# Optimization experiments

Measured on AMD Instinct MI355X. Metric: run time of the kernel, lower is better.

The kernel has to match this reference:

```python
import jax, jax.numpy as jnp
import numpy as np

DIM_EMBED = 256
NUM_DAGS = 1024
OPS_PER_DAG = 100
TOTAL_OPS = NUM_DAGS * OPS_PER_DAG
NUM_WORKERS = 64
H1, H2 = 32, 16


def _mlp_params(key, d_in, scale=0.05):
    ks = jax.random.split(key, 6)
    return dict(
        W1=jax.random.normal(ks[0], (d_in, H1), jnp.float32) * scale,
        b1=jnp.zeros((H1,), jnp.float32),
        W2=jax.random.normal(ks[1], (H1, H2), jnp.float32) * scale,
        b2=jnp.zeros((H2,), jnp.float32),
        W3=jax.random.normal(ks[2], (H2, 1), jnp.float32) * scale,
        b3=jnp.zeros((1,), jnp.float32),
    )


def _mlp(x, W1, b1, W2, b2, W3, b3):
    h = jax.nn.relu(x @ W1 + b1)
    h = jax.nn.relu(h @ W2 + b2)
    return h @ W3 + b3


def setup_inputs() -> dict:
    key = jax.random.key(0)
    k = jax.random.split(key, 8)
    op_p = _mlp_params(k[0], 3 * DIM_EMBED)
    pr_p = _mlp_params(k[1], 2 * DIM_EMBED + 1)
    inp = {
        "num_ops": jnp.full((NUM_DAGS,), OPS_PER_DAG, jnp.int32),
        "num_dags": NUM_DAGS,
        "num_workers": NUM_WORKERS,
        "x": jax.random.normal(k[2], (TOTAL_OPS, DIM_EMBED), jnp.float32),
        "y": jax.random.normal(k[3], (NUM_DAGS, DIM_EMBED), jnp.float32),
        "z": jax.random.normal(k[4], (1, DIM_EMBED), jnp.float32),
        "op_msk": (jax.random.uniform(k[5], (TOTAL_OPS,)) > 0.2).astype(jnp.float32),
        "prlvl_msk": (jax.random.uniform(k[6], (NUM_DAGS, NUM_WORKERS)) > 0.2).astype(jnp.float32),
    }
    for name, p in (("op", op_p), ("pr", pr_p)):
        for pn, pv in p.items():
            inp[f"{name}_{pn}"] = pv
    return inp


def reference(num_ops, num_dags, num_workers, x, y, z, op_msk, prlvl_msk,
              op_W1, op_b1, op_W2, op_b2, op_W3, op_b3,
              pr_W1, pr_b1, pr_W2, pr_b2, pr_W3, pr_b3):
    N = x.shape[0]           # total ops
    D, E = y.shape           # num_dags, dim_embed
    W = num_workers          # python int

    # ---- op branch: repeat_interleave(y, num_ops) == gather by dag id ----
    dag_ids = jnp.repeat(jnp.arange(D), num_ops, total_repeat_length=N)
    ops_feat = jnp.concatenate(
        [x, y[dag_ids], jnp.broadcast_to(z, (N, E))], axis=1)  # [N, 3E]
    ops = _mlp(ops_feat, op_W1, op_b1, op_W2, op_b2, op_W3, op_b3).squeeze(-1)
    ops = ops - (1.0 - op_msk) * 1000.0
    ops = jax.nn.softmax(ops, axis=0)

    # ---- prlvl branch ----
    limits = jnp.arange(1, W + 1, dtype=x.dtype)  # [W]
    feat = jnp.concatenate([
        jnp.broadcast_to(limits[None, :, None], (D, W, 1)),
        jnp.broadcast_to(y[:, None, :], (D, W, E)),
        jnp.broadcast_to(z[None, :, :], (D, W, E)),
    ], axis=-1)  # [D, W, 2E+1]
    prlvl = _mlp(feat, pr_W1, pr_b1, pr_W2, pr_b2, pr_W3, pr_b3).squeeze(-1)
    prlvl = prlvl - (1.0 - prlvl_msk) * 1000.0
    prlvl = jax.nn.softmax(prlvl, axis=1)

    return ops, prlvl
```

## Files before the change

### kernel.cpp

```cpp
#include <hip/hip_runtime.h>
#include <stdint.h>

#define N_OPS 102400
#define NDAG 1024
#define EMB 256

typedef short v8s __attribute__((ext_vector_type(8)));
typedef float v4f __attribute__((ext_vector_type(4)));

__device__ __forceinline__ unsigned short f2bf(float f) {
  union { float f; unsigned int i; } v; v.f = f;
  unsigned int r = v.i + 0x7fffu + ((v.i >> 16) & 1u);
  return (unsigned short)(r >> 16);
}

__global__ __launch_bounds__(256) void k_setup(
    const int* __restrict__ num_ops,
    const float* __restrict__ y, const float* __restrict__ z,
    const float* __restrict__ opW1, const float* __restrict__ opb1,
    const float* __restrict__ opW2,
    const float* __restrict__ prW1, const float* __restrict__ prb1,
    float* __restrict__ ybop, float* __restrict__ ybpr,
    float* __restrict__ zop, float* __restrict__ zpr,
    int* __restrict__ starts,
    unsigned short* __restrict__ wb, unsigned short* __restrict__ wb2)
{
  int t = threadIdx.x;
  int b = blockIdx.x;
  if (b < 512) {
    __shared__ float ylds[512];
    __shared__ float sums[2][2][8][32];
    int d0 = b * 2;
    ylds[t]       = y[d0 * EMB + t];
    ylds[t + 256] = y[d0 * EMB + 256 + t];
    __syncthreads();
    int j = t & 31, p = t >> 5;
    float ao0 = 0, ao1 = 0, ap0 = 0, ap1 = 0;
    for (int k = p * 32; k < p * 32 + 32; ++k) {
      float wo = opW1[(256 + k) * 32 + j];
      float wp = prW1[(1 + k) * 32 + j];
      float y0 = ylds[k];
      float y1 = ylds[256 + k];
      ao0 += y0 * wo; ao1 += y1 * wo;
      ap0 += y0 * wp; ap1 += y1 * wp;
    }
    sums[0][0][p][j] = ao0; sums[1][0][p][j] = ao1;
    sums[0][1][p][j] = ap0; sums[1][1][p][j] = ap1;
    __syncthreads();
    if (t < 128) {
      int j2 = t & 31, g = (t >> 5) & 1, br = t >> 6;
      float s = 0;
      for (int p2 = 0; p2 < 8; ++p2) s += sums[g][br][p2][j2];
      if (br == 0) ybop[(d0 + g) * 32 + j2] = s;
      else         ybpr[(d0 + g) * 32 + j2] = s;
    }
  } else if (b == 512) {
    __shared__ int sc[256];
    int i0 = t * 4;
    int v0 = num_ops[i0], v1 = num_ops[i0 + 1], v2 = num_ops[i0 + 2], v3 = num_ops[i0 + 3];
    int s = v0 + v1 + v2 + v3;
    sc[t] = s;
    __syncthreads();
    for (int off = 1; off < 256; off <<= 1) {
      int tmp = (t >= off) ? sc[t - off] : 0;
      __syncthreads();
      sc[t] += tmp;
      __syncthreads();
    }
    int excl = sc[t] - s;
    starts[i0]     = excl;
    starts[i0 + 1] = excl + v0;
    starts[i0 + 2] = excl + v0 + v1;
    starts[i0 + 3] = excl + v0 + v1 + v2;
    if (t == 255) starts[1024] = sc[255];
  } else {
    __shared__ float zs[2][8][32];
    int j = t & 31, p = t >> 5;
    float aO = 0, aP = 0;
    for (int k = p * 32; k < p * 32 + 32; ++k) {
      float zk = z[k];
      aO += zk * opW1[(512 + k) * 32 + j];
      aP += zk * prW1[(257 + k) * 32 + j];
    }
    zs[0][p][j] = aO; zs[1][p][j] = aP;
    __syncthreads();
    if (t < 64) {
      int j2 = t & 31, br = t >> 5;
      float s = 0;
      for (int p2 = 0; p2 < 8; ++p2) s += zs[br][p2][j2];
      if (br == 0) zop[j2] = s + opb1[j2];
      else         zpr[j2] = s + prb1[j2];
    }
    for (int e = t; e < 8192; e += 256) {
      int j3 = e & 7, l = (e >> 3) & 63, f = (e >> 9) & 1, ks = e >> 10;
      int k = ks * 32 + ((l >> 4) << 3) + j3;
      int col = (l & 15) | (f << 4);
      wb[e] = f2bf(opW1[k * 32 + col]);
    }
    for (int e = t; e < 512; e += 256) {
      int j3 = e & 7, l = e >> 3;
      int k = ((l >> 4) << 3) + j3, n = l & 15;
      wb2[e] = f2bf(opW2[k * 16 + n]);
    }
  }
}

__global__ __launch_bounds__(256) void k_ops(
    const float* __restrict__ x, const float* __restrict__ opmsk,
    const float* __restrict__ opb2, const float* __restrict__ opW3,
    const float* __restrict__ opb3,
    const float* __restrict__ ybop, const float* __restrict__ zop,
    const int* __restrict__ starts,
    const unsigned short* __restrict__ wb, const unsigned short* __restrict__ wb2,
    float* __restrict__ outF, float* __restrict__ bsum)
{
  __shared__ __align__(16) unsigned short h1lds[4][16][40];
  __shared__ float red[4];
  int t = threadIdx.x;
  int wave = t >> 6;
  int l = t & 63;
  int m = l & 15, q = l >> 4;
  int tile = blockIdx.x * 4 + wave;
  int rowBase = tile * 16;

  const v8s* bmat = (const v8s*)wb;
  v4f acc0 = {0, 0, 0, 0}, acc1 = {0, 0, 0, 0};
  const float* xrow = x + (size_t)(rowBase + m) * EMB + q * 8;
#pragma unroll
  for (int ks = 0; ks < 8; ++ks) {
    float4 xa = *(const float4*)(xrow + ks * 32);
    float4 xb = *(const float4*)(xrow + ks * 32 + 4);
    v8s a;
    a[0] = (short)f2bf(xa.x); a[1] = (short)f2bf(xa.y);
    a[2] = (short)f2bf(xa.z); a[3] = (short)f2bf(xa.w);
    a[4] = (short)f2bf(xb.x); a[5] = (short)f2bf(xb.y);
    a[6] = (short)f2bf(xb.z); a[7] = (short)f2bf(xb.w);
    v8s b0 = bmat[(ks * 2 + 0) * 64 + l];
    v8s b1 = bmat[(ks * 2 + 1) * 64 + l];
    acc0 = __builtin_amdgcn_mfma_f32_16x16x32_bf16(a, b0, acc0, 0, 0, 0);
    acc1 = __builtin_amdgcn_mfma_f32_16x16x32_bf16(a, b1, acc1, 0, 0, 0);
  }
  int rr0 = rowBase + q * 4;
  int lo = 0, hi = 1024;
  while (hi - lo > 1) { int mid = (lo + hi) >> 1; if (starts[mid] <= rr0) lo = mid; else hi = mid; }
  int dag = lo;
  float z0 = zop[m], z1 = zop[m + 16];
#pragma unroll
  for (int r = 0; r < 4; ++r) {
    int rr = rr0 + r;
    while (starts[dag + 1] <= rr) ++dag;
    float v0 = acc0[r] + ybop[dag * 32 + m] + z0;
    float v1 = acc1[r] + ybop[dag * 32 + m + 16] + z1;
    v0 = fmaxf(v0, 0.0f); v1 = fmaxf(v1, 0.0f);
    h1lds[wave][q * 4 + r][m]      = f2bf(v0);
    h1lds[wave][q * 4 + r][m + 16] = f2bf(v1);
  }
  __asm__ volatile("s_waitcnt lgkmcnt(0)" ::: "memory");
  v8s a2 = *(const v8s*)(&h1lds[wave][m][q * 8]);
  v8s b2frag = ((const v8s*)wb2)[l];
  v4f zero4 = {0, 0, 0, 0};
  v4f c2 = __builtin_amdgcn_mfma_f32_16x16x32_bf16(a2, b2frag, zero4, 0, 0, 0);

  float b2f = opb2[m];
  float w3f = opW3[m];
  float b3f = opb3[0];
  float sloc = 0.0f;
#pragma unroll
  for (int r = 0; r < 4; ++r) {
    float h2 = fmaxf(c2[r] + b2f, 0.0f);
    float tv = h2 * w3f;
    tv += __shfl_xor(tv, 1, 64);
    tv += __shfl_xor(tv, 2, 64);
    tv += __shfl_xor(tv, 4, 64);
    tv += __shfl_xor(tv, 8, 64);
    if (m == 0) {
      int row = rr0 + r;
      float logit = tv + b3f - 1000.0f * (1.0f - opmsk[row]);
      float e = __expf(logit);
      outF[row] = e;
      sloc += e;
    }
  }
#pragma unroll
  for (int off = 1; off < 64; off <<= 1) sloc += __shfl_xor(sloc, off, 64);
  if (l == 0) red[wave] = sloc;
  __syncthreads();
  if (t == 0) bsum[blockIdx.x] = red[0] + red[1] + red[2] + red[3];
}

__global__ __launch_bounds__(256) void k_final(
    const float* __restrict__ bsum,
    const float* __restrict__ ybpr, const float* __restrict__ zpr,
    const float* __restrict__ prW1, const float* __restrict__ prW2,
    const float* __restrict__ prb2, const float* __restrict__ prW3,
    const float* __restrict__ prb3, const float* __restrict__ prmsk,
    float* __restrict__ outF)
{
  int t = threadIdx.x;
  int b = blockIdx.x;
  if (b < 100) {
    __shared__ float wsum[4];
    int wave = t >> 6, lane = t & 63;
    float s = 0.0f;
    for (int j = t; j < 1600; j += 256) s += bsum[j];
#pragma unroll
    for (int off = 1; off < 64; off <<= 1) s += __shfl_xor(s, off, 64);
    if (lane == 0) wsum[wave] = s;
    __syncthreads();
    float inv = 1.0f / (wsum[0] + wsum[1] + wsum[2] + wsum[3]);
    int i = b * 1024 + t * 4;
    float4 ev = *(const float4*)(outF + i);
    ev.x *= inv; ev.y *= inv; ev.z *= inv; ev.w *= inv;
    *((float4*)(outF + i)) = ev;
  } else {
    int wave = t >> 6, w = t & 63;
    int d = (b - 100) * 4 + wave;
    float h1[32];
    float limit = (float)(w + 1);
#pragma unroll
    for (int j = 0; j < 32; ++j) {
      float base = ybpr[d * 32 + j] + zpr[j];
      h1[j] = fmaxf(base + limit * prW1[j], 0.0f);
    }
    float logit = prb3[0];
#pragma unroll
    for (int n = 0; n < 16; ++n) {
      float acc = prb2[n];
#pragma unroll
      for (int j = 0; j < 32; ++j) acc += h1[j] * prW2[j * 16 + n];
      logit += fmaxf(acc, 0.0f) * prW3[n];
    }
    logit -= 1000.0f * (1.0f - prmsk[d * 64 + w]);
    float mx = logit;
#pragma unroll
    for (int off = 1; off < 64; off <<= 1) mx = fmaxf(mx, __shfl_xor(mx, off, 64));
    float e = __expf(logit - mx);
    float s = e;
#pragma unroll
    for (int off = 1; off < 64; off <<= 1) s += __shfl_xor(s, off, 64);
    outF[N_OPS + d * 64 + w] = e / s;
  }
}

extern "C" void kernel_launch(void* const* d_in, const int* in_sizes, int n_in,
                              void* d_out, int out_size, void* d_ws, size_t ws_size,
                              hipStream_t stream) {
  const int* num_ops = (const int*)d_in[0];
  const float* x     = (const float*)d_in[3];
  const float* y     = (const float*)d_in[4];
  const float* z     = (const float*)d_in[5];
  const float* opmsk = (const float*)d_in[6];
  const float* prmsk = (const float*)d_in[7];
  const float* opW1 = (const float*)d_in[8];
  const float* opb1 = (const float*)d_in[9];
  const float* opW2 = (const float*)d_in[10];
  const float* opb2 = (const float*)d_in[11];
  const float* opW3 = (const float*)d_in[12];
  const float* opb3 = (const float*)d_in[13];
  const float* prW1 = (const float*)d_in[14];
  const float* prb1 = (const float*)d_in[15];
  const float* prW2 = (const float*)d_in[16];
  const float* prb2 = (const float*)d_in[17];
  const float* prW3 = (const float*)d_in[18];
  const float* prb3 = (const float*)d_in[19];

  char* ws = (char*)d_ws;
  float* ybop  = (float*)(ws + 0);
  float* ybpr  = (float*)(ws + 131072);
  float* zop   = (float*)(ws + 262144);
  float* zpr   = (float*)(ws + 262272);
  int*   starts= (int*)  (ws + 262400);
  unsigned short* wb  = (unsigned short*)(ws + 267008);
  unsigned short* wb2 = (unsigned short*)(ws + 283392);
  float* bsum  = (float*)(ws + 284416);
  float* outF  = (float*)d_out;

  hipLaunchKernelGGL(k_setup, dim3(514), dim3(256), 0, stream,
      num_ops, y, z, opW1, opb1, opW2, prW1, prb1,
      ybop, ybpr, zop, zpr, starts, wb, wb2);
  hipLaunchKernelGGL(k_ops, dim3(1600), dim3(256), 0, stream,
      x, opmsk, opb2, opW3, opb3, ybop, zop, starts, wb, wb2, outF, bsum);
  hipLaunchKernelGGL(k_final, dim3(356), dim3(256), 0, stream,
      bsum, ybpr, zpr, prW1, prW2, prb2, prW3, prb3, prmsk, outF);
}
```

Baseline: 232.0 us.

## Fuse setup into main ops kernel with per-block redundant prologue computation

Merges the setup kernel into the ops and prlvl kernels, producing two launches in place of three. Each block now recomputes the num_ops prefix scan, the bf16 weight swizzle into LDS, the z projection and the per-dag y projections it needs. This removes one launch and the global round-trips for intermediate buffers. In exchange every one of the 1856 blocks does redundant prologue work (a 1024-entry scan, 8K weight conversions, several dependent GEMV rounds separated by syncs) and uses more LDS, which may lower occupancy.

```diff
diff --git a/kernel.cpp b/kernel.cpp
--- a/kernel.cpp
+++ b/kernel.cpp
@@ -14,220 +14,208 @@
   return (unsigned short)(r >> 16);
 }
 
-__global__ __launch_bounds__(256) void k_setup(
+__global__ __launch_bounds__(256) void k_main(
     const int* __restrict__ num_ops,
-    const float* __restrict__ y, const float* __restrict__ z,
+    const float* __restrict__ x, const float* __restrict__ y,
+    const float* __restrict__ z,
+    const float* __restrict__ opmsk, const float* __restrict__ prmsk,
     const float* __restrict__ opW1, const float* __restrict__ opb1,
-    const float* __restrict__ opW2,
+    const float* __restrict__ opW2, const float* __restrict__ opb2,
+    const float* __restrict__ opW3, const float* __restrict__ opb3,
     const float* __restrict__ prW1, const float* __restrict__ prb1,
-    float* __restrict__ ybop, float* __restrict__ ybpr,
-    float* __restrict__ zop, float* __restrict__ zpr,
-    int* __restrict__ starts,
-    unsigned short* __restrict__ wb, unsigned short* __restrict__ wb2)
+    const float* __restrict__ prW2, const float* __restrict__ prb2,
+    const float* __restrict__ prW3, const float* __restrict__ prb3,
+    float* __restrict__ bsum, float* __restrict__ outF)
 {
-  int t = threadIdx.x;
-  int b = blockIdx.x;
-  if (b < 512) {
-    __shared__ float ylds[512];
-    __shared__ float sums[2][2][8][32];
-    int d0 = b * 2;
-    ylds[t]       = y[d0 * EMB + t];
-    ylds[t + 256] = y[d0 * EMB + 256 + t];
-    __syncthreads();
-    int j = t & 31, p = t >> 5;
-    float ao0 = 0, ao1 = 0, ap0 = 0, ap1 = 0;
-    for (int k = p * 32; k < p * 32 + 32; ++k) {
-      float wo = opW1[(256 + k) * 32 + j];
-      float wp = prW1[(1 + k) * 32 + j];
-      float y0 = ylds[k];
-      float y1 = ylds[256 + k];
-      ao0 += y0 * wo; ao1 += y1 * wo;
-      ap0 += y0 * wp; ap1 += y1 * wp;
-    }
-    sums[0][0][p][j] = ao0; sums[1][0][p][j] = ao1;
-    sums[0][1][p][j] = ap0; sums[1][1][p][j] = ap1;
-    __syncthreads();
-    if (t < 128) {
-      int j2 = t & 31, g = (t >> 5) & 1, br = t >> 6;
-      float s = 0;
-      for (int p2 = 0; p2 < 8; ++p2) s += sums[g][br][p2][j2];
-      if (br == 0) ybop[(d0 + g) * 32 + j2] = s;
-      else         ybpr[(d0 + g) * 32 + j2] = s;
-    }
-  } else if (b == 512) {
-    __shared__ int sc[256];
-    int i0 = t * 4;
-    int v0 = num_ops[i0], v1 = num_ops[i0 + 1], v2 = num_ops[i0 + 2], v3 = num_ops[i0 + 3];
-    int s = v0 + v1 + v2 + v3;
-    sc[t] = s;
-    __syncthreads();
-    for (int off = 1; off < 256; off <<= 1) {
-      int tmp = (t >= off) ? sc[t - off] : 0;
-      __syncthreads();
-      sc[t] += tmp;
-      __syncthreads();
-    }
-    int excl = sc[t] - s;
-    starts[i0]     = excl;
-    starts[i0 + 1] = excl + v0;
-    starts[i0 + 2] = excl + v0 + v1;
-    starts[i0 + 3] = excl + v0 + v1 + v2;
-    if (t == 255) starts[1024] = sc[255];
-  } else {
-    __shared__ float zs[2][8][32];
-    int j = t & 31, p = t >> 5;
-    float aO = 0, aP = 0;
-    for (int k = p * 32; k < p * 32 + 32; ++k) {
-      float zk = z[k];
-      aO += zk * opW1[(512 + k) * 32 + j];
-      aP += zk * prW1[(257 + k) * 32 + j];
-    }
-    zs[0][p][j] = aO; zs[1][p][j] = aP;
-    __syncthreads();
-    if (t < 64) {
-      int j2 = t & 31, br = t >> 5;
-      float s = 0;
-      for (int p2 = 0; p2 < 8; ++p2) s += zs[br][p2][j2];
-      if (br == 0) zop[j2] = s + opb1[j2];
-      else         zpr[j2] = s + prb1[j2];
+  __shared__ int st[1025];
+  __shared__ int sc[256];
+  __shared__ float sums[8][32];
+  __shared__ float biasL[17][32];
+  __shared__ float zL[32];
+  __shared__ float limW[32];
+  __shared__ __align__(16) unsigned short wbL[8192];
+  __shared__ __align__(16) unsigned short wb2L[512];
+  __shared__ __align__(16) unsigned short h1lds[4][16][40];
+  __shared__ float red[4];
+
+  int t = threadIdx.x, b = blockIdx.x;
+  int j = t & 31, p = t >> 5;
+
+  if (b < 1600) {
+    {
+      int i0 = t * 4;
+      int v0 = num_ops[i0], v1 = num_ops[i0 + 1];
+      int v2 = num_ops[i0 + 2], v3 = num_ops[i0 + 3];
+      int s = v0 + v1 + v2 + v3;
+      sc[t] = s;
+      __syncthreads();
+      for (int off = 1; off < 256; off <<= 1) {
+        int tmp = (t >= off) ? sc[t - off] : 0;
+        __syncthreads();
+        sc[t] += tmp;
+        __syncthreads();
+      }
+      int excl = sc[t] - s;
+      st[i0]     = excl;
+      st[i0 + 1] = excl + v0;
+      st[i0 + 2] = excl + v0 + v1;
+      st[i0 + 3] = excl + v0 + v1 + v2;
+      if (t == 255) st[1024] = sc[255];
     }
     for (int e = t; e < 8192; e += 256) {
       int j3 = e & 7, l = (e >> 3) & 63, f = (e >> 9) & 1, ks = e >> 10;
       int k = ks * 32 + ((l >> 4) << 3) + j3;
       int col = (l & 15) | (f << 4);
-      wb[e] = f2bf(opW1[k * 32 + col]);
+      wbL[e] = f2bf(opW1[k * 32 + col]);
     }
     for (int e = t; e < 512; e += 256) {
       int j3 = e & 7, l = e >> 3;
       int k = ((l >> 4) << 3) + j3, n = l & 15;
-      wb2[e] = f2bf(opW2[k * 16 + n]);
-    }
-  }
-}
-
-__global__ __launch_bounds__(256) void k_ops(
-    const float* __restrict__ x, const float* __restrict__ opmsk,
-    const float* __restrict__ opb2, const float* __restrict__ opW3,
-    const float* __restrict__ opb3,
-    const float* __restrict__ ybop, const float* __restrict__ zop,
-    const int* __restrict__ starts,
-    const unsigned short* __restrict__ wb, const unsigned short* __restrict__ wb2,
-    float* __restrict__ outF, float* __restrict__ bsum)
-{
-  __shared__ __align__(16) unsigned short h1lds[4][16][40];
-  __shared__ float red[4];
-  int t = threadIdx.x;
-  int wave = t >> 6;
-  int l = t & 63;
-  int m = l & 15, q = l >> 4;
-  int tile = blockIdx.x * 4 + wave;
-  int rowBase = tile * 16;
-
-  const v8s* bmat = (const v8s*)wb;
-  v4f acc0 = {0, 0, 0, 0}, acc1 = {0, 0, 0, 0};
-  const float* xrow = x + (size_t)(rowBase + m) * EMB + q * 8;
-#pragma unroll
-  for (int ks = 0; ks < 8; ++ks) {
-    float4 xa = *(const float4*)(xrow + ks * 32);
-    float4 xb = *(const float4*)(xrow + ks * 32 + 4);
-    v8s a;
-    a[0] = (short)f2bf(xa.x); a[1] = (short)f2bf(xa.y);
-    a[2] = (short)f2bf(xa.z); a[3] = (short)f2bf(xa.w);
-    a[4] = (short)f2bf(xb.x); a[5] = (short)f2bf(xb.y);
-    a[6] = (short)f2bf(xb.z); a[7] = (short)f2bf(xb.w);
-    v8s b0 = bmat[(ks * 2 + 0) * 64 + l];
-    v8s b1 = bmat[(ks * 2 + 1) * 64 + l];
-    acc0 = __builtin_amdgcn_mfma_f32_16x16x32_bf16(a, b0, acc0, 0, 0, 0);
-    acc1 = __builtin_amdgcn_mfma_f32_16x16x32_bf16(a, b1, acc1, 0, 0, 0);
-  }
-  int rr0 = rowBase + q * 4;
-  int lo = 0, hi = 1024;
-  while (hi - lo > 1) { int mid = (lo + hi) >> 1; if (starts[mid] <= rr0) lo = mid; else hi = mid; }
-  int dag = lo;
-  float z0 = zop[m], z1 = zop[m + 16];
-#pragma unroll
-  for (int r = 0; r < 4; ++r) {
-    int rr = rr0 + r;
-    while (starts[dag + 1] <= rr) ++dag;
-    float v0 = acc0[r] + ybop[dag * 32 + m] + z0;
-    float v1 = acc1[r] + ybop[dag * 32 + m + 16] + z1;
-    v0 = fmaxf(v0, 0.0f); v1 = fmaxf(v1, 0.0f);
-    h1lds[wave][q * 4 + r][m]      = f2bf(v0);
-    h1lds[wave][q * 4 + r][m + 16] = f2bf(v1);
-  }
-  __asm__ volatile("s_waitcnt lgkmcnt(0)" ::: "memory");
-  v8s a2 = *(const v8s*)(&h1lds[wave][m][q * 8]);
-  v8s b2frag = ((const v8s*)wb2)[l];
-  v4f zero4 = {0, 0, 0, 0};
-  v4f c2 = __builtin_amdgcn_mfma_f32_16x16x32_bf16(a2, b2frag, zero4, 0, 0, 0);
-
-  float b2f = opb2[m];
-  float w3f = opW3[m];
-  float b3f = opb3[0];
-  float sloc = 0.0f;
-#pragma unroll
-  for (int r = 0; r < 4; ++r) {
-    float h2 = fmaxf(c2[r] + b2f, 0.0f);
-    float tv = h2 * w3f;
-    tv += __shfl_xor(tv, 1, 64);
-    tv += __shfl_xor(tv, 2, 64);
-    tv += __shfl_xor(tv, 4, 64);
-    tv += __shfl_xor(tv, 8, 64);
-    if (m == 0) {
-      int row = rr0 + r;
-      float logit = tv + b3f - 1000.0f * (1.0f - opmsk[row]);
-      float e = __expf(logit);
-      outF[row] = e;
-      sloc += e;
-    }
-  }
-#pragma unroll
-  for (int off = 1; off < 64; off <<= 1) sloc += __shfl_xor(sloc, off, 64);
-  if (l == 0) red[wave] = sloc;
-  __syncthreads();
-  if (t == 0) bsum[blockIdx.x] = red[0] + red[1] + red[2] + red[3];
-}
-
-__global__ __launch_bounds__(256) void k_final(
-    const float* __restrict__ bsum,
-    const float* __restrict__ ybpr, const float* __restrict__ zpr,
-    const float* __restrict__ prW1, const float* __restrict__ prW2,
-    const float* __restrict__ prb2, const float* __restrict__ prW3,
-    const float* __restrict__ prb3, const float* __restrict__ prmsk,
-    float* __restrict__ outF)
-{
-  int t = threadIdx.x;
-  int b = blockIdx.x;
-  if (b < 100) {
-    __shared__ float wsum[4];
-    int wave = t >> 6, lane = t & 63;
-    float s = 0.0f;
-    for (int j = t; j < 1600; j += 256) s += bsum[j];
-#pragma unroll
-    for (int off = 1; off < 64; off <<= 1) s += __shfl_xor(s, off, 64);
-    if (lane == 0) wsum[wave] = s;
-    __syncthreads();
-    float inv = 1.0f / (wsum[0] + wsum[1] + wsum[2] + wsum[3]);
-    int i = b * 1024 + t * 4;
-    float4 ev = *(const float4*)(outF + i);
-    ev.x *= inv; ev.y *= inv; ev.z *= inv; ev.w *= inv;
-    *((float4*)(outF + i)) = ev;
+      wb2L[e] = f2bf(opW2[k * 16 + n]);
+    }
+    {
+      float a = 0;
+      for (int k = p * 32; k < p * 32 + 32; ++k) a += z[k] * opW1[(512 + k) * 32 + j];
+      sums[p][j] = a;
+    }
+    __syncthreads();
+    if (t < 32) {
+      float s2 = 0;
+      for (int q2 = 0; q2 < 8; ++q2) s2 += sums[q2][t];
+      zL[t] = s2 + opb1[t];
+    }
+    __syncthreads();
+    int rowBase = b * 64;
+    int lo = 0, hi = 1024;
+    while (hi - lo > 1) { int mid = (lo + hi) >> 1; if (st[mid] <= rowBase) lo = mid; else hi = mid; }
+    int dagF = lo;
+    lo = dagF; hi = 1024;
+    while (hi - lo > 1) { int mid = (lo + hi) >> 1; if (st[mid] <= rowBase + 63) lo = mid; else hi = mid; }
+    int nd = lo - dagF + 1;
+    if (nd > 17) nd = 17;
+    for (int dl = 0; dl < nd; ++dl) {
+      int dag = dagF + dl;
+      const float* yr = y + (size_t)dag * EMB;
+      float a = 0;
+      for (int k = p * 32; k < p * 32 + 32; ++k) a += yr[k] * opW1[(256 + k) * 32 + j];
+      sums[p][j] = a;
+      __syncthreads();
+      if (t < 32) {
+        float s2 = 0;
+        for (int q2 = 0; q2 < 8; ++q2) s2 += sums[q2][t];
+        biasL[dl][t] = s2;
+      }
+      __syncthreads();
+    }
+
+    int wave = t >> 6, l = t & 63;
+    int m = l & 15, q = l >> 4;
+    int rowB = rowBase + wave * 16;
+    const v8s* bmat = (const v8s*)wbL;
+    v4f acc0 = {0, 0, 0, 0}, acc1 = {0, 0, 0, 0};
+    const float* xrow = x + (size_t)(rowB + m) * EMB + q * 8;
+#pragma unroll
+    for (int ks = 0; ks < 8; ++ks) {
+      float4 xa = *(const float4*)(xrow + ks * 32);
+      float4 xb = *(const float4*)(xrow + ks * 32 + 4);
+      v8s a;
+      a[0] = (short)f2bf(xa.x); a[1] = (short)f2bf(xa.y);
+      a[2] = (short)f2bf(xa.z); a[3] = (short)f2bf(xa.w);
+      a[4] = (short)f2bf(xb.x); a[5] = (short)f2bf(xb.y);
+      a[6] = (short)f2bf(xb.z); a[7] = (short)f2bf(xb.w);
+      v8s b0 = bmat[(ks * 2 + 0) * 64 + l];
+      v8s b1 = bmat[(ks * 2 + 1) * 64 + l];
+      acc0 = __builtin_amdgcn_mfma_f32_16x16x32_bf16(a, b0, acc0, 0, 0, 0);
+      acc1 = __builtin_amdgcn_mfma_f32_16x16x32_bf16(a, b1, acc1, 0, 0, 0);
+    }
+    int rr0 = rowB + q * 4;
+    int dag = dagF;
+    while (dag < 1023 && st[dag + 1] <= rr0) ++dag;
+    float z0 = zL[m], z1 = zL[m + 16];
+#pragma unroll
+    for (int r = 0; r < 4; ++r) {
+      int rr = rr0 + r;
+      while (dag < 1023 && st[dag + 1] <= rr) ++dag;
+      int di = dag - dagF; if (di > 16) di = 16;
+      float v0 = acc0[r] + biasL[di][m] + z0;
+      float v1 = acc1[r] + biasL[di][m + 16] + z1;
+      v0 = fmaxf(v0, 0.0f); v1 = fmaxf(v1, 0.0f);
+      h1lds[wave][q * 4 + r][m]      = f2bf(v0);
+      h1lds[wave][q * 4 + r][m + 16] = f2bf(v1);
+    }
+    __asm__ volatile("s_waitcnt lgkmcnt(0)" ::: "memory");
+    v8s a2 = *(const v8s*)(&h1lds[wave][m][q * 8]);
+    v8s b2frag = ((const v8s*)wb2L)[l];
+    v4f zero4 = {0, 0, 0, 0};
+    v4f c2 = __builtin_amdgcn_mfma_f32_16x16x32_bf16(a2, b2frag, zero4, 0, 0, 0);
+
+    float b2f = opb2[m];
+    float w3f = opW3[m];
+    float b3f = opb3[0];
+    float sloc = 0.0f;
+#pragma unroll
+    for (int r = 0; r < 4; ++r) {
+      float h2 = fmaxf(c2[r] + b2f, 0.0f);
+      float tv = h2 * w3f;
+      tv += __shfl_xor(tv, 1, 64);
+      tv += __shfl_xor(tv, 2, 64);
+      tv += __shfl_xor(tv, 4, 64);
+      tv += __shfl_xor(tv, 8, 64);
+      if (m == 0) {
+        int row = rr0 + r;
+        float logit = tv + b3f - 1000.0f * (1.0f - opmsk[row]);
+        float e = __expf(logit);
+        outF[row] = e;
+        sloc += e;
+      }
+    }
+#pragma unroll
+    for (int off = 1; off < 64; off <<= 1) sloc += __shfl_xor(sloc, off, 64);
+    if (l == 0) red[wave] = sloc;
+    __syncthreads();
+    if (t == 0) bsum[b] = red[0] + red[1] + red[2] + red[3];
+
   } else {
+    int d0 = (b - 1600) * 4;
+    {
+      float a = 0;
+      for (int k = p * 32; k < p * 32 + 32; ++k) a += z[k] * prW1[(257 + k) * 32 + j];
+      sums[p][j] = a;
+    }
+    __syncthreads();
+    if (t < 32) {
+      float s2 = 0;
+      for (int q2 = 0; q2 < 8; ++q2) s2 += sums[q2][t];
+      zL[t] = s2 + prb1[t];
+    }
+    if (t >= 32 && t < 64) limW[t - 32] = prW1[t - 32];
+    __syncthreads();
+    for (int dl = 0; dl < 4; ++dl) {
+      const float* yr = y + (size_t)(d0 + dl) * EMB;
+      float a = 0;
+      for (int k = p * 32; k < p * 32 + 32; ++k) a += yr[k] * prW1[(1 + k) * 32 + j];
+      sums[p][j] = a;
+      __syncthreads();
+      if (t < 32) {
+        float s2 = 0;
+        for (int q2 = 0; q2 < 8; ++q2) s2 += sums[q2][t];
+        biasL[dl][t] = s2;
+      }
+      __syncthreads();
+    }
     int wave = t >> 6, w = t & 63;
-    int d = (b - 100) * 4 + wave;
+    int d = d0 + wave;
     float h1[32];
     float limit = (float)(w + 1);
 #pragma unroll
-    for (int j = 0; j < 32; ++j) {
-      float base = ybpr[d * 32 + j] + zpr[j];
-      h1[j] = fmaxf(base + limit * prW1[j], 0.0f);
-    }
+    for (int j2 = 0; j2 < 32; ++j2)
+      h1[j2] = fmaxf(biasL[wave][j2] + zL[j2] + limit * limW[j2], 0.0f);
     float logit = prb3[0];
 #pragma unroll
     for (int n = 0; n < 16; ++n) {
       float acc = prb2[n];
 #pragma unroll
-      for (int j = 0; j < 32; ++j) acc += h1[j] * prW2[j * 16 + n];
+      for (int j2 = 0; j2 < 32; ++j2) acc += h1[j2] * prW2[j2 * 16 + n];
       logit += fmaxf(acc, 0.0f) * prW3[n];
     }
     logit -= 1000.0f * (1.0f - prmsk[d * 64 + w]);
@@ -240,6 +228,25 @@
     for (int off = 1; off < 64; off <<= 1) s += __shfl_xor(s, off, 64);
     outF[N_OPS + d * 64 + w] = e / s;
   }
+}
+
+__global__ __launch_bounds__(256) void k_norm(const float* __restrict__ bsum,
+                                              float* __restrict__ outF)
+{
+  __shared__ float wsum[4];
+  int t = threadIdx.x, b = blockIdx.x;
+  int wave = t >> 6, lane = t & 63;
+  float s = 0.0f;
+  for (int i = t; i < 1600; i += 256) s += bsum[i];
+#pragma unroll
+  for (int off = 1; off < 64; off <<= 1) s += __shfl_xor(s, off, 64);
+  if (lane == 0) wsum[wave] = s;
+  __syncthreads();
+  float inv = 1.0f / (wsum[0] + wsum[1] + wsum[2] + wsum[3]);
+  int i = b * 1024 + t * 4;
+  float4 ev = *(const float4*)(outF + i);
+  ev.x *= inv; ev.y *= inv; ev.z *= inv; ev.w *= inv;
+  *((float4*)(outF + i)) = ev;
 }
 
 extern "C" void kernel_launch(void* const* d_in, const int* in_sizes, int n_in,
@@ -264,22 +271,13 @@
   const float* prW3 = (const float*)d_in[18];
   const float* prb3 = (const float*)d_in[19];
 
-  char* ws = (char*)d_ws;
-  float* ybop  = (float*)(ws + 0);
-  float* ybpr  = (float*)(ws + 131072);
-  float* zop   = (float*)(ws + 262144);
-  float* zpr   = (float*)(ws + 262272);
-  int*   starts= (int*)  (ws + 262400);
-  unsigned short* wb  = (unsigned short*)(ws + 267008);
-  unsigned short* wb2 = (unsigned short*)(ws + 283392);
-  float* bsum  = (float*)(ws + 284416);
-  float* outF  = (float*)d_out;
-
-  hipLaunchKernelGGL(k_setup, dim3(514), dim3(256), 0, stream,
-      num_ops, y, z, opW1, opb1, opW2, prW1, prb1,
-      ybop, ybpr, zop, zpr, starts, wb, wb2);
-  hipLaunchKernelGGL(k_ops, dim3(1600), dim3(256), 0, stream,
-      x, opmsk, opb2, opW3, opb3, ybop, zop, starts, wb, wb2, outF, bsum);
-  hipLaunchKernelGGL(k_final, dim3(356), dim3(256), 0, stream,
-      bsum, ybpr, zpr, prW1, prW2, prb2, prW3, prb3, prmsk, outF);
-}
+  float* bsum = (float*)d_ws;
+  float* outF = (float*)d_out;
+
+  hipLaunchKernelGGL(k_main, dim3(1856), dim3(256), 0, stream,
+      num_ops, x, y, z, opmsk, prmsk,
+      opW1, opb1, opW2, opb2, opW3, opb3,
+      prW1, prb1, prW2, prb2, prW3, prb3,
+      bsum, outF);
+  hipLaunchKernelGGL(k_norm, dim3(100), dim3(256), 0, stream, bsum, outF);
+}
```

Result: no change. 232.5 us (+0.2%).
